# Kernel tuning notes

Hardware: AMD Instinct MI355X
Metric: run time of the kernel (lower is better)

Reference implementation:

```python
import jax, jax.numpy as jnp
import numpy as np

B, T, D, H, L, E, K, FF, V = 2, 1024, 1024, 16, 3, 8, 2, 4096, 32000
HD = D // H


def _rmsnorm(x):
    return x * jax.lax.rsqrt(jnp.mean(x * x, axis=-1, keepdims=True) + 1e-5)


def _forward(idx, wte, wpe, wq, wk, wv, wo, gate, f1, f2, lm_head):
    Bc, Tc = idx.shape
    x = wte[idx] + wpe[:Tc]            # (B,T,D)
    x = _rmsnorm(x)
    causal = jnp.tril(jnp.ones((Tc, Tc), dtype=bool))
    total_aux = jnp.zeros((), dtype=x.dtype)
    scale = 1.0 / np.sqrt(HD)
    for l in range(L):
        xr = x
        xn = _rmsnorm(x)
        q = (xn @ wq[l].T).reshape(Bc, Tc, H, HD).transpose(0, 2, 1, 3)
        k = (xn @ wk[l].T).reshape(Bc, Tc, H, HD).transpose(0, 2, 1, 3)
        v = (xn @ wv[l].T).reshape(Bc, Tc, H, HD).transpose(0, 2, 1, 3)
        att = jnp.einsum('bhqd,bhkd->bhqk', q, k) * scale
        att = jnp.where(causal, att, -jnp.inf)
        att = jax.nn.softmax(att, axis=-1)
        o = jnp.einsum('bhqk,bhkd->bhqd', att, v)
        o = o.transpose(0, 2, 1, 3).reshape(Bc, Tc, D)
        x = o @ wo[l].T + xr
        # MoE FFN (dense compute over all experts, gather top-k)
        xr = x
        xn = _rmsnorm(x)
        gate_probs = jax.nn.softmax(jnp.einsum('btd,ed->bte', xn, gate[l]), axis=-1)
        topk_vals, topk_idx = jax.lax.top_k(gate_probs, K)   # (B,T,K)
        topk_w = topk_vals / topk_vals.sum(axis=-1, keepdims=True)
        h = jax.nn.relu(jnp.einsum('btd,efd->btef', xn, f1[l]))  # (B,T,E,FF)
        expert_stack = jnp.einsum('btef,edf->bted', h, f2[l])    # (B,T,E,D)
        selected = jnp.take_along_axis(expert_stack, topk_idx[..., None], axis=2)  # (B,T,K,D)
        moe_out = (selected * topk_w[..., None]).sum(axis=2)
        frac = gate_probs.mean(axis=(0, 1))
        total_aux = total_aux + E * jnp.sum(frac * frac)
        x = moe_out + xr
    logits = x @ lm_head.T              # (B,T,V)
    aux_loss = 0.01 * total_aux / L
    return logits, aux_loss


def setup_inputs() -> dict:
    key = jax.random.key(0)
    ks = jax.random.split(key, 12)
    s = 0.02
    return {
        'idx': jax.random.randint(ks[0], (B, T), 0, V, dtype=jnp.int64) if jax.config.jax_enable_x64 else jax.random.randint(ks[0], (B, T), 0, V, dtype=jnp.int32),
        'wte': jax.random.normal(ks[1], (V, D), jnp.float32) * s,
        'wpe': jax.random.normal(ks[2], (T, D), jnp.float32) * s,
        'wq': jax.random.normal(ks[3], (L, D, D), jnp.float32) * s,
        'wk': jax.random.normal(ks[4], (L, D, D), jnp.float32) * s,
        'wv': jax.random.normal(ks[5], (L, D, D), jnp.float32) * s,
        'wo': jax.random.normal(ks[6], (L, D, D), jnp.float32) * s,
        'gate': jax.random.normal(ks[7], (L, E, D), jnp.float32) * s,
        'f1': jax.random.normal(ks[8], (L, E, FF, D), jnp.float32) * s,
        'f2': jax.random.normal(ks[9], (L, E, D, FF), jnp.float32) * s,
        'lm_head': jax.random.normal(ks[10], (V, D), jnp.float32) * s,
    }


def reference(idx, wte, wpe, wq, wk, wv, wo, gate, f1, f2, lm_head):
    return _forward(idx, wte, wpe, wq, wk, wv, wo, gate, f1, f2, lm_head)
```

## Files before the change

kernel.cpp:

```cpp
#include <hip/hip_runtime.h>

typedef unsigned short u16;
typedef __attribute__((ext_vector_type(4))) float f32x4;
typedef __attribute__((ext_vector_type(8))) __bf16 bf16x8;
typedef __attribute__((ext_vector_type(8))) _Float16 f16x8;
typedef __attribute__((ext_vector_type(4))) unsigned short u16x4;
typedef __attribute__((ext_vector_type(8))) unsigned short u16x8;

constexpr int kT = 1024, kD = 1024, kH = 16, kHD = 64, kL = 3, kE = 8;
constexpr int kFF = 4096, kV = 32000, kBT = 2048, kSLOTS = 5120;

__device__ __forceinline__ u16 f2bf(float f) {
  union { float f; unsigned u; } v; v.f = f;
  unsigned r = v.u + 0x7FFFu + ((v.u >> 16) & 1u);
  return (u16)(r >> 16);
}
__device__ __forceinline__ u16 f2h(float x) {
  _Float16 h = (_Float16)x;
  union { _Float16 h; u16 u; } v; v.h = h; return v.u;
}
__device__ __forceinline__ void split2s(float x, u16& h, u16& m) {
  float xs = x * 64.0f;
  _Float16 hh = (_Float16)xs;
  union { _Float16 h; u16 u; } v; v.h = hh; h = v.u;
  float r = xs - (float)hh;
  union { _Float16 h; u16 u; } w; w.h = (_Float16)r; m = w.u;
}

__device__ __forceinline__ void ld_lds16(const void* g, void* l) {
  __builtin_amdgcn_global_load_lds((const __attribute__((address_space(1))) void*)g,
                                   (__attribute__((address_space(3))) void*)l, 16, 0, 0);
}

#define MFMA16(a, b, c) __builtin_amdgcn_mfma_f32_16x16x32_bf16(a, b, c, 0, 0, 0)
#define MFMAH(a, b, c)  __builtin_amdgcn_mfma_f32_16x16x32_f16(a, b, c, 0, 0, 0)

__device__ __forceinline__ float blockReduceSum256(float v) {
  #pragma unroll
  for (int m = 32; m >= 1; m >>= 1) v += __shfl_xor(v, m);
  __shared__ float sh_[4];
  int w = threadIdx.x >> 6;
  if ((threadIdx.x & 63) == 0) sh_[w] = v;
  __syncthreads();
  v = (sh_[0] + sh_[1]) + (sh_[2] + sh_[3]);
  __syncthreads();
  return v;
}


__global__ __launch_bounds__(256) void cast_bf16_k(const float* __restrict__ in,
                                                   u16* __restrict__ out, long n4) {
  long i = (long)blockIdx.x * 256 + threadIdx.x;
  long stride = (long)gridDim.x * 256;
  for (; i < n4; i += stride) {
    f32x4 v = ((const f32x4*)in)[i];
    u16x4 o; o[0] = f2bf(v[0]); o[1] = f2bf(v[1]); o[2] = f2bf(v[2]); o[3] = f2bf(v[3]);
    ((u16x4*)out)[i] = o;
  }
}

__global__ __launch_bounds__(256) void cast_h_k(const float* __restrict__ in,
                                                u16* __restrict__ out, long n4) {
  long i = (long)blockIdx.x * 256 + threadIdx.x;
  long stride = (long)gridDim.x * 256;
  for (; i < n4; i += stride) {
    f32x4 v = ((const f32x4*)in)[i];
    u16x4 o; o[0] = f2h(v[0]); o[1] = f2h(v[1]); o[2] = f2h(v[2]); o[3] = f2h(v[3]);
    ((u16x4*)out)[i] = o;
  }
}

__global__ __launch_bounds__(256) void split2h_k(const float* __restrict__ in,
    u16* __restrict__ out, long planeStride, long n4) {
  long i = (long)blockIdx.x * 256 + threadIdx.x;
  long stride = (long)gridDim.x * 256;
  u16* o1 = out + planeStride;
  for (; i < n4; i += stride) {
    f32x4 v = ((const f32x4*)in)[i];
    u16x4 a, b;
    #pragma unroll
    for (int j = 0; j < 4; ++j) {
      u16 h, m; split2s(v[j], h, m);
      a[j] = h; b[j] = m;
    }
    ((u16x4*)out)[i] = a; ((u16x4*)o1)[i] = b;
  }
}

__global__ __launch_bounds__(256) void qkvcomb_k(const float* __restrict__ a,
    const float* __restrict__ b, u16* __restrict__ oP, long plane, long n4) {
  long i = (long)blockIdx.x * 256 + threadIdx.x;
  long stride = (long)gridDim.x * 256;
  for (; i < n4; i += stride) {
    f32x4 v = ((const f32x4*)a)[i] + ((const f32x4*)b)[i];
    u16x4 hh, mm;
    #pragma unroll
    for (int j = 0; j < 4; ++j) {
      u16 h, m; split2s(v[j], h, m);
      hh[j] = h; mm[j] = m;
    }
    ((u16x4*)oP)[i] = hh;
    ((u16x4*)(oP + plane))[i] = mm;
  }
}

__global__ __launch_bounds__(256) void embed_rms_k(const int* __restrict__ idx,
    const float* __restrict__ wte, const float* __restrict__ wpe, float* __restrict__ x) {
  int tok = blockIdx.x, t = threadIdx.x;
  int id = idx[tok];
  int tt = tok & (kT - 1);
  f32x4 a = ((const f32x4*)(wte + (long)id * kD))[t];
  f32x4 p = ((const f32x4*)(wpe + (long)tt * kD))[t];
  f32x4 vv = a + p;
  float ss = vv[0]*vv[0] + vv[1]*vv[1] + vv[2]*vv[2] + vv[3]*vv[3];
  ss = blockReduceSum256(ss);
  float sc = rsqrtf(ss * (1.0f / kD) + 1e-5f);
  vv *= sc;
  ((f32x4*)(x + (long)tok * kD))[t] = vv;
}

__global__ __launch_bounds__(256) void rmsnorm2_k(const float* __restrict__ x,
    float* __restrict__ xnf, u16* __restrict__ xnb) {
  int tok = blockIdx.x, t = threadIdx.x;
  f32x4 vv = ((const f32x4*)(x + (long)tok * kD))[t];
  float ss = blockReduceSum256(vv[0]*vv[0] + vv[1]*vv[1] + vv[2]*vv[2] + vv[3]*vv[3]);
  float sc = rsqrtf(ss * (1.0f / kD) + 1e-5f);
  vv *= sc;
  ((f32x4*)(xnf + (long)tok * kD))[t] = vv;
  u16x4 o;
  o[0] = f2bf(vv[0]); o[1] = f2bf(vv[1]); o[2] = f2bf(vv[2]); o[3] = f2bf(vv[3]);
  ((u16x4*)(xnb + (long)tok * kD))[t] = o;
}

__global__ __launch_bounds__(256) void rmsnorm2h_k(const float* __restrict__ x,
    u16* __restrict__ xnP, long plane) {
  int tok = blockIdx.x, t = threadIdx.x;
  f32x4 vv = ((const f32x4*)(x + (long)tok * kD))[t];
  float ss = blockReduceSum256(vv[0]*vv[0] + vv[1]*vv[1] + vv[2]*vv[2] + vv[3]*vv[3]);
  float sc = rsqrtf(ss * (1.0f / kD) + 1e-5f);
  vv *= sc;
  u16x4 a, b;
  #pragma unroll
  for (int j = 0; j < 4; ++j) {
    u16 h, m; split2s(vv[j], h, m);
    a[j] = h; b[j] = m;
  }
  long o = (long)tok * kD / 4 + t;
  ((u16x4*)xnP)[o] = a;
  ((u16x4*)(xnP + plane))[o] = b;
}

__global__ __launch_bounds__(256) void resid4_rms2h_k(float* __restrict__ x,
    const float* __restrict__ parts, long plane, u16* __restrict__ xnP, long xplane) {
  int tok = blockIdx.x, t = threadIdx.x;
  long o = (long)tok * (kD / 4) + t;
  f32x4 xv = ((f32x4*)x)[o];
  #pragma unroll
  for (int p = 0; p < 4; ++p) xv += ((const f32x4*)(parts + p * plane))[o];
  ((f32x4*)x)[o] = xv;
  float ss = blockReduceSum256(xv[0]*xv[0] + xv[1]*xv[1] + xv[2]*xv[2] + xv[3]*xv[3]);
  float sc = rsqrtf(ss * (1.0f / kD) + 1e-5f);
  f32x4 vv = xv * sc;
  u16x4 a, b;
  #pragma unroll
  for (int j = 0; j < 4; ++j) {
    u16 h, m; split2s(vv[j], h, m);
    a[j] = h; b[j] = m;
  }
  ((u16x4*)xnP)[o] = a;
  ((u16x4*)(xnP + xplane))[o] = b;
}

__global__ __launch_bounds__(256) void moe4_rms2h_k(float* __restrict__ x,
    const float* __restrict__ outsP, long plane, const int* __restrict__ slotOf,
    const float* __restrict__ top2w, u16* __restrict__ xnP, long xplane) {
  int tok = blockIdx.x, t = threadIdx.x;
  int s0 = slotOf[tok*2], s1 = slotOf[tok*2+1];
  float w0 = top2w[tok*2], w1 = top2w[tok*2+1];
  f32x4 a = {0.f,0.f,0.f,0.f}, b = a;
  #pragma unroll
  for (int p = 0; p < 4; ++p) {
    a += ((const f32x4*)(outsP + p * plane + (long)s0 * kD))[t];
    b += ((const f32x4*)(outsP + p * plane + (long)s1 * kD))[t];
  }
  long o = (long)tok * (kD / 4) + t;
  f32x4 xv = ((f32x4*)x)[o];
  xv += a * w0 + b * w1;
  ((f32x4*)x)[o] = xv;
  float ss = blockReduceSum256(xv[0]*xv[0] + xv[1]*xv[1] + xv[2]*xv[2] + xv[3]*xv[3]);
  float sc = rsqrtf(ss * (1.0f / kD) + 1e-5f);
  f32x4 vv = xv * sc;
  u16x4 ha, hb;
  #pragma unroll
  for (int j = 0; j < 4; ++j) {
    u16 h, m; split2s(vv[j], h, m);
    ha[j] = h; hb[j] = m;
  }
  ((u16x4*)xnP)[o] = ha;
  ((u16x4*)(xnP + xplane))[o] = hb;
}

__global__ __launch_bounds__(256) void moe4_cast_h_k(float* __restrict__ x,
    const float* __restrict__ outsP, long plane, const int* __restrict__ slotOf,
    const float* __restrict__ top2w, u16* __restrict__ xn) {
  int tok = blockIdx.x, t = threadIdx.x;
  int s0 = slotOf[tok*2], s1 = slotOf[tok*2+1];
  float w0 = top2w[tok*2], w1 = top2w[tok*2+1];
  f32x4 a = {0.f,0.f,0.f,0.f}, b = a;
  #pragma unroll
  for (int p = 0; p < 4; ++p) {
    a += ((const f32x4*)(outsP + p * plane + (long)s0 * kD))[t];
    b += ((const f32x4*)(outsP + p * plane + (long)s1 * kD))[t];
  }
  long o = (long)tok * (kD / 4) + t;
  f32x4 xv = ((f32x4*)x)[o];
  xv += a * w0 + b * w1;
  u16x4 hv;
  #pragma unroll
  for (int j = 0; j < 4; ++j) hv[j] = f2h(xv[j]);
  ((u16x4*)xn)[o] = hv;
}

__global__ __launch_bounds__(256) void gate_topk_k(const float* __restrict__ x,
    const float* __restrict__ gate_l, float* __restrict__ probs, int* __restrict__ top2e,
    float* __restrict__ top2w, int* __restrict__ counts) {
  int tok = blockIdx.x, t = threadIdx.x;
  f32x4 xv = ((const f32x4*)(x + (long)tok * kD))[t];
  float ss = blockReduceSum256(xv[0]*xv[0] + xv[1]*xv[1] + xv[2]*xv[2] + xv[3]*xv[3]);
  float sc = rsqrtf(ss * (1.0f / kD) + 1e-5f);
  float a[kE];
  #pragma unroll
  for (int e = 0; e < kE; ++e) {
    f32x4 gv = ((const f32x4*)(gate_l + (long)e * kD))[t];
    a[e] = xv[0]*gv[0] + xv[1]*gv[1] + xv[2]*gv[2] + xv[3]*gv[3];
  }
  __shared__ float sh8[kE][4];
  int w = t >> 6, l = t & 63;
  #pragma unroll
  for (int e = 0; e < kE; ++e) {
    float v = a[e];
    #pragma unroll
    for (int m = 32; m >= 1; m >>= 1) v += __shfl_xor(v, m);
    if (l == 0) sh8[e][w] = v;
  }
  __syncthreads();
  if (t == 0) {
    float lg[kE], mx = -1e30f;
    #pragma unroll
    for (int e = 0; e < kE; ++e) {
      lg[e] = (sh8[e][0] + sh8[e][1] + sh8[e][2] + sh8[e][3]) * sc;
      mx = fmaxf(mx, lg[e]);
    }
    float pe[kE], s = 0.f;
    #pragma unroll
    for (int e = 0; e < kE; ++e) { pe[e] = __expf(lg[e] - mx); s += pe[e]; }
    float inv = 1.f / s;
    int i1 = 0;
    #pragma unroll
    for (int e = 1; e < kE; ++e) if (lg[e] > lg[i1]) i1 = e;
    int i2 = (i1 == 0) ? 1 : 0;
    #pragma unroll
    for (int e = 0; e < kE; ++e) if (e != i1 && lg[e] > lg[i2]) i2 = e;
    #pragma unroll
    for (int e = 0; e < kE; ++e) probs[(long)tok * kE + e] = pe[e] * inv;
    float p1 = pe[i1] * inv, p2 = pe[i2] * inv;
    float wn = p1 + p2;
    top2e[tok*2] = i1; top2e[tok*2+1] = i2;
    top2w[tok*2] = p1 / wn; top2w[tok*2+1] = p2 / wn;
    atomicAdd(&counts[i1], 1); atomicAdd(&counts[i2], 1);
  }
}

__global__ void calc_offsets_k(const int* __restrict__ counts, int* __restrict__ offsets) {
  if (threadIdx.x == 0) {
    int o = 0;
    #pragma unroll
    for (int e = 0; e < kE; ++e) { offsets[e] = o; o += (counts[e] + 127) & ~127; }
    offsets[kE] = o;
  }
}

__global__ __launch_bounds__(256) void fill_slots_k(const int* __restrict__ top2e,
    const int* __restrict__ offsets, int* __restrict__ cursors,
    int* __restrict__ rows, int* __restrict__ slotOf) {
  int tok = blockIdx.x * 256 + threadIdx.x;
  if (tok >= kBT) return;
  #pragma unroll
  for (int j = 0; j < 2; ++j) {
    int e = top2e[tok*2 + j];
    int pos = atomicAdd(&cursors[e], 1);
    int slot = offsets[e] + pos;
    rows[slot] = tok;
    slotOf[tok*2 + j] = slot;
  }
}

__global__ __launch_bounds__(256) void moe_combine4_k(float* __restrict__ x,
    const float* __restrict__ outsP, long plane, const int* __restrict__ slotOf,
    const float* __restrict__ top2w) {
  int tok = blockIdx.x, t = threadIdx.x;
  int s0 = slotOf[tok*2], s1 = slotOf[tok*2+1];
  float w0 = top2w[tok*2], w1 = top2w[tok*2+1];
  f32x4 a = {0.f,0.f,0.f,0.f}, b = a;
  #pragma unroll
  for (int p = 0; p < 4; ++p) {
    a += ((const f32x4*)(outsP + p * plane + (long)s0 * kD))[t];
    b += ((const f32x4*)(outsP + p * plane + (long)s1 * kD))[t];
  }
  f32x4 xv = ((f32x4*)(x + (long)tok * kD))[t];
  xv += a * w0 + b * w1;
  ((f32x4*)(x + (long)tok * kD))[t] = xv;
}

__global__ __launch_bounds__(256) void aux_reduce_k(const float* __restrict__ probs,
                                                    float* __restrict__ aux) {
  int t = threadIdx.x;
  float part[kE] = {};
  for (int i = t; i < kBT; i += 256) {
    #pragma unroll
    for (int e = 0; e < kE; ++e) part[e] += probs[(long)i * kE + e];
  }
  __shared__ float sh8[kE][4];
  int w = t >> 6, l = t & 63;
  #pragma unroll
  for (int e = 0; e < kE; ++e) {
    float v = part[e];
    #pragma unroll
    for (int m = 32; m >= 1; m >>= 1) v += __shfl_xor(v, m);
    if (l == 0) sh8[e][w] = v;
  }
  __syncthreads();
  if (t == 0) {
    float acc = 0.f;
    #pragma unroll
    for (int e = 0; e < kE; ++e) {
      float frac = (sh8[e][0] + sh8[e][1] + sh8[e][2] + sh8[e][3]) * (1.0f / kBT);
      acc += frac * frac;
    }
    aux[0] += (float)kE * acc;
  }
}

__global__ void write_aux_k(const float* __restrict__ aux, float* __restrict__ out) {
  if (threadIdx.x == 0) out[0] = 0.01f * aux[0] / (float)kL;
}

enum { P_BF16 = 0, P_BF16_RELU = 1, P_F32 = 2, P_F32_RESID = 3, P_F32_RELU = 4,
       P_SPLIT2_RELU = 5, P_F16_RELU = 6 };

__device__ __forceinline__ int clamp_row(int rv) {
  return ((unsigned)rv < (unsigned)kBT) ? rv : 0;
}

template <bool MPART>
__device__ __forceinline__ void block_mn(int lin, int base, int mArg, int& mb, int& nb) {
  int xcd = lin & 7, c = lin >> 3;
  if (MPART) {
    mb = xcd * mArg + (c % mArg);
    nb = c / mArg;
  } else {
    int swz = xcd * (base >> 3) + c;
    mb = swz % mArg;
    nb = swz / mArg;
  }
}


template <int POST, bool GATHER, bool EXPERT, bool MPART, bool BF32>
__global__ __launch_bounds__(256) void gemm2h_bt_k(
    const u16* __restrict__ A0, long planeA,
    const void* __restrict__ Bv, long planeB,
    void* __restrict__ C, long planeC,
    const float* __restrict__ resid,
    const int* __restrict__ rows, const int* __restrict__ offsets,
    int N, int K, int lda, long eBstride, int mArg,
    int kParts, int base, long cPart) {
  constexpr int BM = 128, BK = 32;
  int part = blockIdx.x / base;
  int lin = blockIdx.x % base;
  int mb, nb;
  block_mn<MPART>(lin, base, mArg, mb, nb);
  int m0 = mb * BM, n0 = nb * BM;
  const u16* B0 = (const u16*)Bv;
  const float* Bf = (const float*)Bv;
  if (EXPERT) {
    int total = offsets[kE];
    if (m0 >= total) return;
    int e = 0;
    while (offsets[e + 1] <= m0) ++e;
    if (BF32) Bf += (long)e * eBstride; else B0 += (long)e * eBstride;
  }
  __shared__ __align__(16) u16 Ac[BM][64];
  __shared__ __align__(16) u16 Bc[BM][64];
  int t = threadIdx.x;
  int l = t & 63, lr = l & 15, lg = l >> 4;
  int wid = t >> 6;
  int wm = (wid >> 1) * 64, wn = (wid & 1) * 64;

  long asrc[4], bsrc[4];
  int ldst[4];
  #pragma unroll
  for (int it = 0; it < 4; ++it) {
    int d = it * 256 + t;
    int row = d >> 3, pc = d & 7;
    int lc = pc ^ (row & 7);
    int p = lc >> 2, c = lc & 3;
    int grow = GATHER ? clamp_row(rows[m0 + row]) : (m0 + row);
    asrc[it] = (long)p * planeA + (long)grow * lda + c * 8;
    if (!BF32) bsrc[it] = (long)p * planeB + (long)(n0 + row) * K + c * 8;
    ldst[it] = (it * 256 + (t & ~63)) * 8;
  }
  long bsrcF[2];
  int brow[2], bc[2];
  if (BF32) {
    #pragma unroll
    for (int it = 0; it < 2; ++it) {
      int d = it * 256 + t;
      brow[it] = d >> 2; bc[it] = d & 3;
      bsrcF[it] = (long)(n0 + brow[it]) * K + bc[it] * 8;
    }
  }
  int sa = lr & 7;
  int cH = (lg ^ sa) * 8;
  int cM = ((4 + lg) ^ sa) * 8;

  f32x4 acc[4][4];
  #pragma unroll
  for (int i = 0; i < 4; ++i)
    #pragma unroll
    for (int j = 0; j < 4; ++j) acc[i][j] = 0.f;

  int kStep = K / kParts;
  int kLo = part * kStep, kHi = kLo + kStep;
  for (int k0 = kLo; k0 < kHi; k0 += BK) {
    #pragma unroll
    for (int it = 0; it < 4; ++it) {
      ld_lds16(A0 + asrc[it] + k0, &Ac[0][0] + ldst[it]);
      if (!BF32) ld_lds16(B0 + bsrc[it] + k0, &Bc[0][0] + ldst[it]);
    }
    if (BF32) {
      #pragma unroll
      for (int it = 0; it < 2; ++it) {
        const float* src = Bf + bsrcF[it] + k0;
        f32x4 v0 = *(const f32x4*)src;
        f32x4 v1 = *(const f32x4*)(src + 4);
        u16x8 hi, mi;
        #pragma unroll
        for (int j = 0; j < 4; ++j) {
          u16 h, m; split2s(v0[j], h, m); hi[j] = h; mi[j] = m;
        }
        #pragma unroll
        for (int j = 0; j < 4; ++j) {
          u16 h, m; split2s(v1[j], h, m); hi[4 + j] = h; mi[4 + j] = m;
        }
        int r7 = brow[it] & 7;
        *(u16x8*)&Bc[brow[it]][(bc[it] ^ r7) * 8] = hi;
        *(u16x8*)&Bc[brow[it]][((4 + bc[it]) ^ r7) * 8] = mi;
      }
    }
    __syncthreads();
    f16x8 ah[4], am[4];
    #pragma unroll
    for (int i = 0; i < 4; ++i) {
      ah[i] = *(const f16x8*)&Ac[wm + i*16 + lr][cH];
      am[i] = *(const f16x8*)&Ac[wm + i*16 + lr][cM];
    }
    #pragma unroll
    for (int j = 0; j < 4; ++j) {
      f16x8 bh = *(const f16x8*)&Bc[wn + j*16 + lr][cH];
      f16x8 bm = *(const f16x8*)&Bc[wn + j*16 + lr][cM];
      #pragma unroll
      for (int i = 0; i < 4; ++i) {
        acc[i][j] = MFMAH(ah[i], bh, acc[i][j]);
        acc[i][j] = MFMAH(am[i], bh, acc[i][j]);
        acc[i][j] = MFMAH(ah[i], bm, acc[i][j]);
      }
    }
    __syncthreads();
  }
  float* Cf = (float*)C + (long)part * cPart;
  #pragma unroll
  for (int i = 0; i < 4; ++i) {
    #pragma unroll
    for (int r = 0; r < 4; ++r) {
      long m = m0 + wm + i*16 + lg*4 + r;
      #pragma unroll
      for (int j = 0; j < 4; ++j) {
        int n = n0 + wn + j*16 + lr;
        float val = acc[i][j][r] * (1.0f / 4096.0f);
        if (POST == P_F32) {
          Cf[m * N + n] = val;
        } else if (POST == P_F32_RESID) {
          ((float*)C)[m * N + n] = val + resid[m * N + n];
        } else if (POST == P_SPLIT2_RELU) {
          val = fmaxf(val, 0.f);
          u16 h, mm; split2s(val, h, mm);
          u16* Cp = (u16*)C;
          Cp[m * N + n] = h;
          Cp[planeC + m * N + n] = mm;
        }
      }
    }
  }
}


template <int POST, bool GATHER, bool EXPERT, bool BF32>
__global__ __launch_bounds__(512) void gemm2hW_bt_k(
    const u16* __restrict__ A0, long planeA,
    const void* __restrict__ Bv, long planeB,
    void* __restrict__ C, long planeC,
    const int* __restrict__ rows, const int* __restrict__ offsets,
    int N, int K, int lda, long eBstride, int mPerX,
    int kParts, int base, long cPart) {
  constexpr int BM = 128, BN = 256, BK = 32;
  int part = blockIdx.x / base;
  int lin = blockIdx.x % base;
  int xcd = lin & 7, c0 = lin >> 3;
  int m0 = (xcd * mPerX + (c0 % mPerX)) * BM;
  int n0 = (c0 / mPerX) * BN;
  const u16* B0 = (const u16*)Bv;
  const float* Bf = (const float*)Bv;
  if (EXPERT) {
    int total = offsets[kE];
    if (m0 >= total) return;
    int e = 0;
    while (offsets[e + 1] <= m0) ++e;
    if (BF32) Bf += (long)e * eBstride; else B0 += (long)e * eBstride;
  }
  __shared__ __align__(16) u16 Ac[BM][64];
  __shared__ __align__(16) u16 Bc[BN][64];
  int t = threadIdx.x;
  int l = t & 63, lr = l & 15, lg = l >> 4;
  int wid = t >> 6;
  int wm = (wid >> 2) * 64;
  int wn = (wid & 3) * 64;

  long asrc[2], bsrc[4];
  int aldst[2], bldst[4];
  #pragma unroll
  for (int it = 0; it < 2; ++it) {
    int d = it * 512 + t;
    int row = d >> 3, pc = d & 7;
    int lc = pc ^ (row & 7);
    int p = lc >> 2, cc = lc & 3;
    int grow = GATHER ? clamp_row(rows[m0 + row]) : (m0 + row);
    asrc[it] = (long)p * planeA + (long)grow * lda + cc * 8;
    aldst[it] = (it * 512 + (t & ~63)) * 8;
  }
  long bsrcF[2];
  int brow[2], bcc[2];
  if (!BF32) {
    #pragma unroll
    for (int it = 0; it < 4; ++it) {
      int d = it * 512 + t;
      int row = d >> 3, pc = d & 7;
      int lc = pc ^ (row & 7);
      int p = lc >> 2, cc = lc & 3;
      bsrc[it] = (long)p * planeB + (long)(n0 + row) * K + cc * 8;
      bldst[it] = (it * 512 + (t & ~63)) * 8;
    }
  } else {
    #pragma unroll
    for (int it = 0; it < 2; ++it) {
      int d = it * 512 + t;
      brow[it] = d >> 2; bcc[it] = d & 3;
      bsrcF[it] = (long)(n0 + brow[it]) * K + bcc[it] * 8;
    }
  }
  int sa = lr & 7;
  int cH = (lg ^ sa) * 8;
  int cM = ((4 + lg) ^ sa) * 8;

  f32x4 acc[4][4];
  #pragma unroll
  for (int i = 0; i < 4; ++i)
    #pragma unroll
    for (int j = 0; j < 4; ++j) acc[i][j] = 0.f;

  int kStep = K / kParts;
  int kLo = part * kStep, kHi = kLo + kStep;
  for (int k0 = kLo; k0 < kHi; k0 += BK) {
    #pragma unroll
    for (int it = 0; it < 2; ++it)
      ld_lds16(A0 + asrc[it] + k0, &Ac[0][0] + aldst[it]);
    if (!BF32) {
      #pragma unroll
      for (int it = 0; it < 4; ++it)
        ld_lds16(B0 + bsrc[it] + k0, &Bc[0][0] + bldst[it]);
    } else {
      #pragma unroll
      for (int it = 0; it < 2; ++it) {
        const float* src = Bf + bsrcF[it] + k0;
        f32x4 v0 = *(const f32x4*)src;
        f32x4 v1 = *(const f32x4*)(src + 4);
        u16x8 hi, mi;
        #pragma unroll
        for (int j = 0; j < 4; ++j) {
          u16 h, m; split2s(v0[j], h, m); hi[j] = h; mi[j] = m;
        }
        #pragma unroll
        for (int j = 0; j < 4; ++j) {
          u16 h, m; split2s(v1[j], h, m); hi[4 + j] = h; mi[4 + j] = m;
        }
        int r7 = brow[it] & 7;
        *(u16x8*)&Bc[brow[it]][(bcc[it] ^ r7) * 8] = hi;
        *(u16x8*)&Bc[brow[it]][((4 + bcc[it]) ^ r7) * 8] = mi;
      }
    }
    __syncthreads();
    f16x8 ah[4], am[4];
    #pragma unroll
    for (int i = 0; i < 4; ++i) {
      ah[i] = *(const f16x8*)&Ac[wm + i*16 + lr][cH];
      am[i] = *(const f16x8*)&Ac[wm + i*16 + lr][cM];
    }
    #pragma unroll
    for (int j = 0; j < 4; ++j) {
      f16x8 bh = *(const f16x8*)&Bc[wn + j*16 + lr][cH];
      f16x8 bm = *(const f16x8*)&Bc[wn + j*16 + lr][cM];
      #pragma unroll
      for (int i = 0; i < 4; ++i) {
        acc[i][j] = MFMAH(ah[i], bh, acc[i][j]);
        acc[i][j] = MFMAH(am[i], bh, acc[i][j]);
        acc[i][j] = MFMAH(ah[i], bm, acc[i][j]);
      }
    }
    __syncthreads();
  }
  float* Cf = (float*)C + (long)part * cPart;
  #pragma unroll
  for (int i = 0; i < 4; ++i) {
    #pragma unroll
    for (int r = 0; r < 4; ++r) {
      long m = m0 + wm + i*16 + lg*4 + r;
      #pragma unroll
      for (int j = 0; j < 4; ++j) {
        int n = n0 + wn + j*16 + lr;
        float val = acc[i][j][r] * (1.0f / 4096.0f);
        if (POST == P_F32) {
          Cf[m * N + n] = val;
        } else if (POST == P_SPLIT2_RELU) {
          val = fmaxf(val, 0.f);
          u16 h, mm; split2s(val, h, mm);
          u16* Cp = (u16*)C;
          Cp[m * N + n] = h;
          Cp[planeC + m * N + n] = mm;
        }
      }
    }
  }
}


template <int POST, bool EXPERT, bool GATHER, bool HALF, bool BCONV, bool MPART>
__global__ __launch_bounds__(256) void gemm_bt_k(
    const u16* __restrict__ A, const void* __restrict__ Bv, void* __restrict__ C,
    const int* __restrict__ rows, const int* __restrict__ offsets,
    int N, int K, int lda, long eBstride, float oscale, int mArg,
    int kParts, int base, long cPart) {
  constexpr int BM = 128, BK = 64;
  int part = blockIdx.x / base;
  int lin = blockIdx.x % base;
  int mb, nb;
  block_mn<MPART>(lin, base, mArg, mb, nb);
  int m0 = mb * BM, n0 = nb * BM;
  const float* Bf = (const float*)Bv;
  const u16*   Bh = (const u16*)Bv;
  if (EXPERT) {
    int total = offsets[kE];
    if (m0 >= total) return;
    int e = 0;
    while (offsets[e + 1] <= m0) ++e;
    if (BCONV) Bf += (long)e * eBstride; else Bh += (long)e * eBstride;
  }
  __shared__ __align__(16) u16 As[BM][BK];
  __shared__ __align__(16) u16 Bs[BM][BK + (BCONV ? 8 : 0)];
  int t = threadIdx.x;
  int l = t & 63, lr = l & 15, lg = l >> 4;
  int wid = t >> 6;
  int wm = (wid >> 1) * 64, wn = (wid & 1) * 64;

  long asrc[4], bsrc[4];
  int ldst[4];
  #pragma unroll
  for (int it = 0; it < 4; ++it) {
    int d = it * 256 + t;
    int row = d >> 3, pc = d & 7;
    int c = pc ^ (row & 7);
    int grow = GATHER ? clamp_row(rows[m0 + row]) : (m0 + row);
    asrc[it] = (long)grow * lda + c * 8;
    bsrc[it] = (long)(n0 + row) * K + c * 8;
    ldst[it] = (it * 256 + (t & ~63)) * 8;
  }
  f32x4 acc[4][4];
  #pragma unroll
  for (int i = 0; i < 4; ++i)
    #pragma unroll
    for (int j = 0; j < 4; ++j) acc[i][j] = 0.f;

  int kStep = K / kParts;
  int kLo = part * kStep, kHi = kLo + kStep;
  for (int k0 = kLo; k0 < kHi; k0 += BK) {
    #pragma unroll
    for (int it = 0; it < 4; ++it)
      ld_lds16(A + asrc[it] + k0, &As[0][0] + ldst[it]);
    if (!BCONV) {
      #pragma unroll
      for (int it = 0; it < 4; ++it)
        ld_lds16(Bh + bsrc[it] + k0, &Bs[0][0] + ldst[it]);
    } else {
      #pragma unroll
      for (int it = 0; it < 8; ++it) {
        int c = it * 256 + t;
        int row = c >> 4, col = (c & 15) * 4;
        f32x4 v = *(const f32x4*)(Bf + (long)(n0 + row) * K + k0 + col);
        u16x4 o;
        #pragma unroll
        for (int j = 0; j < 4; ++j) o[j] = HALF ? f2h(v[j]) : f2bf(v[j]);
        *(u16x4*)&Bs[row][col] = o;
      }
    }
    __syncthreads();
    #pragma unroll
    for (int kk = 0; kk < 2; ++kk) {
      int ca = ((kk * 4 + lg) ^ (lr & 7)) * 8;
      int cb = BCONV ? (kk * 32 + lg * 8) : ca;
      #pragma unroll
      for (int i = 0; i < 4; ++i)
        #pragma unroll
        for (int j = 0; j < 4; ++j) {
          if (HALF) {
            f16x8 af = *(const f16x8*)&As[wm + i*16 + lr][ca];
            f16x8 bq = *(const f16x8*)&Bs[wn + j*16 + lr][cb];
            acc[i][j] = MFMAH(af, bq, acc[i][j]);
          } else {
            bf16x8 af = *(const bf16x8*)&As[wm + i*16 + lr][ca];
            bf16x8 bq = *(const bf16x8*)&Bs[wn + j*16 + lr][cb];
            acc[i][j] = MFMA16(af, bq, acc[i][j]);
          }
        }
    }
    __syncthreads();
  }
  #pragma unroll
  for (int i = 0; i < 4; ++i) {
    #pragma unroll
    for (int r = 0; r < 4; ++r) {
      long m = m0 + wm + i*16 + lg*4 + r;
      #pragma unroll
      for (int j = 0; j < 4; ++j) {
        int n = n0 + wn + j*16 + lr;
        float val = acc[i][j][r] * oscale;
        if (POST == P_BF16_RELU)       ((u16*)C)[m * N + n] = f2bf(fmaxf(val, 0.f));
        else if (POST == P_F16_RELU)   ((u16*)C)[m * N + n] = f2h(fmaxf(val, 0.f));
        else if (POST == P_F32)        ((float*)C + (long)part * cPart)[m * N + n] = val;
      }
    }
  }
}


template <int POST, bool GATHER, bool EXPERT>
__global__ __launch_bounds__(256) void sgemm_bt_k(
    const float* __restrict__ A, const float* __restrict__ B, float* __restrict__ C,
    const float* __restrict__ resid, const int* __restrict__ rows,
    const int* __restrict__ offsets, int N, int K, int lda, long eBstride) {
  constexpr int BM = 128, BN = 128, BK = 32;
  int m0 = blockIdx.x * BM, n0 = blockIdx.y * BN;
  if (EXPERT) {
    int total = offsets[kE];
    if (m0 >= total) return;
    int e = 0;
    while (offsets[e + 1] <= m0) ++e;
    B += (long)e * eBstride;
  }
  __shared__ float Ast[BK][BM];
  __shared__ float Bst[BK][BN];
  int t = threadIdx.x, tx = t & 15, ty = t >> 4;
  long asrc[4], bsrc[4];
  #pragma unroll
  for (int it = 0; it < 4; ++it) {
    int c = it * 256 + t;
    int row = c >> 3, kc = (c & 7) * 4;
    int gr = GATHER ? clamp_row(rows[m0 + row]) : (m0 + row);
    asrc[it] = (long)gr * lda + kc;
    bsrc[it] = (long)(n0 + row) * K + kc;
  }
  f32x4 accv[8][2];
  #pragma unroll
  for (int i = 0; i < 8; ++i) { accv[i][0] = 0.f; accv[i][1] = 0.f; }

  for (int k0 = 0; k0 < K; k0 += BK) {
    #pragma unroll
    for (int it = 0; it < 4; ++it) {
      int c = it * 256 + t;
      int row = c >> 3, kc = (c & 7) * 4;
      f32x4 av = *(const f32x4*)(A + asrc[it] + k0);
      f32x4 bv = *(const f32x4*)(B + bsrc[it] + k0);
      #pragma unroll
      for (int j = 0; j < 4; ++j) { Ast[kc + j][row] = av[j]; Bst[kc + j][row] = bv[j]; }
    }
    __syncthreads();
    #pragma unroll
    for (int kk = 0; kk < BK; ++kk) {
      f32x4 a0 = *(const f32x4*)&Ast[kk][ty * 4];
      f32x4 a1 = *(const f32x4*)&Ast[kk][64 + ty * 4];
      f32x4 b0 = *(const f32x4*)&Bst[kk][tx * 4];
      f32x4 b1 = *(const f32x4*)&Bst[kk][64 + tx * 4];
      float as[8] = {a0[0], a0[1], a0[2], a0[3], a1[0], a1[1], a1[2], a1[3]};
      #pragma unroll
      for (int i = 0; i < 8; ++i) {
        accv[i][0] += b0 * as[i];
        accv[i][1] += b1 * as[i];
      }
    }
    __syncthreads();
  }
  #pragma unroll
  for (int ih = 0; ih < 2; ++ih)
    #pragma unroll
    for (int i = 0; i < 4; ++i) {
      long m = m0 + ih * 64 + ty * 4 + i;
      #pragma unroll
      for (int jh = 0; jh < 2; ++jh) {
        long n = n0 + jh * 64 + tx * 4;
        f32x4 val = accv[ih * 4 + i][jh];
        if (POST == P_F32_RELU) {
          #pragma unroll
          for (int j = 0; j < 4; ++j) val[j] = fmaxf(val[j], 0.f);
        }
        if (POST == P_F32_RESID) val += *(const f32x4*)&resid[m * N + n];
        *(f32x4*)&C[m * N + n] = val;
      }
    }
}


__global__ __launch_bounds__(256) void attn2h_k(
    const u16* __restrict__ qkvP, long qplane,
    u16* __restrict__ oP, long oplane) {
  int qt = (int)gridDim.x - 1 - (int)blockIdx.x;
  int bh = blockIdx.y;
  int b = bh >> 4, h = bh & 15;
  const int ldq = 3 * kD;
  long hbq = (long)b * kT * ldq + h * kHD;
  long hbo = (long)b * kT * kD + h * kHD;
  int t = threadIdx.x, w = t >> 6, l = t & 63;
  int lr = l & 15, lg = l >> 4;

  __shared__ __align__(16) u16 Ks[2][64][72];
  __shared__ __align__(16) u16 Vt[2][64][72];
  __shared__ __align__(16) u16 Ps[2][4][16][72];

  f16x8 qf0[2], qf1[2];
  {
    long qrow = qt * 64 + w * 16 + lr;
    const u16* qp = qkvP + hbq + qrow * ldq;
    #pragma unroll
    for (int kc = 0; kc < 2; ++kc) {
      qf0[kc] = *(const f16x8*)(qp + kc * 32 + lg * 8);
      qf1[kc] = *(const f16x8*)(qp + qplane + kc * 32 + lg * 8);
    }
  }
  int qg = qt * 64 + w * 16 + lg * 4;

  float mrow[4], lsum[4];
  f32x4 accO[4];
  #pragma unroll
  for (int r = 0; r < 4; ++r) { mrow[r] = -1e30f; lsum[r] = 0.f; }
  #pragma unroll
  for (int j = 0; j < 4; ++j) accO[j] = 0.f;

  for (int it = 0; it <= qt; ++it) {
    #pragma unroll
    for (int p = 0; p < 2; ++p) {
      #pragma unroll
      for (int s = 0; s < 2; ++s) {
        int c = s * 256 + t;
        int row = c >> 3, col = (c & 7) * 8;
        long gi = (long)p * qplane + hbq + (long)(it * 64 + row) * ldq + col;
        *(u16x8*)&Ks[p][row][col] = *(const u16x8*)(qkvP + kD + gi);
        u16x8 vv = *(const u16x8*)(qkvP + 2 * kD + gi);
        #pragma unroll
        for (int j = 0; j < 8; ++j) Vt[p][col + j][row] = vv[j];
      }
    }
    __syncthreads();

    f32x4 s4[4];
    #pragma unroll
    for (int j = 0; j < 4; ++j) {
      f32x4 z = {0.f, 0.f, 0.f, 0.f};
      #pragma unroll
      for (int kc = 0; kc < 2; ++kc) {
        f16x8 kh = *(const f16x8*)&Ks[0][j*16 + lr][kc*32 + lg*8];
        f16x8 km = *(const f16x8*)&Ks[1][j*16 + lr][kc*32 + lg*8];
        z = MFMAH(qf0[kc], kh, z);
        z = MFMAH(qf1[kc], kh, z);
        z = MFMAH(qf0[kc], km, z);
      }
      s4[j] = z;
    }
    #pragma unroll
    for (int j = 0; j < 4; ++j)
      #pragma unroll
      for (int r = 0; r < 4; ++r) {
        float sv = s4[j][r] * (0.125f / 4096.0f);
        if (it * 64 + j * 16 + lr > qg + r) sv = -1e30f;
        s4[j][r] = sv;
      }
    float alpha[4];
    #pragma unroll
    for (int r = 0; r < 4; ++r) {
      float mx = fmaxf(fmaxf(s4[0][r], s4[1][r]), fmaxf(s4[2][r], s4[3][r]));
      mx = fmaxf(mx, __shfl_xor(mx, 1));
      mx = fmaxf(mx, __shfl_xor(mx, 2));
      mx = fmaxf(mx, __shfl_xor(mx, 4));
      mx = fmaxf(mx, __shfl_xor(mx, 8));
      float mi = fmaxf(mrow[r], mx);
      alpha[r] = __expf(mrow[r] - mi);
      mrow[r] = mi;
    }
    float rs[4] = {0.f, 0.f, 0.f, 0.f};
    #pragma unroll
    for (int j = 0; j < 4; ++j)
      #pragma unroll
      for (int r = 0; r < 4; ++r) {
        float p = __expf(s4[j][r] - mrow[r]);
        rs[r] += p;
        u16 hh, mm; split2s(p, hh, mm);
        Ps[0][w][lg*4 + r][j*16 + lr] = hh;
        Ps[1][w][lg*4 + r][j*16 + lr] = mm;
      }
    #pragma unroll
    for (int r = 0; r < 4; ++r) {
      float x2 = rs[r];
      x2 += __shfl_xor(x2, 1);
      x2 += __shfl_xor(x2, 2);
      x2 += __shfl_xor(x2, 4);
      x2 += __shfl_xor(x2, 8);
      lsum[r] = lsum[r] * alpha[r] + x2;
    }
    #pragma unroll
    for (int j = 0; j < 4; ++j)
      #pragma unroll
      for (int r = 0; r < 4; ++r) accO[j][r] *= alpha[r];
    __syncthreads();

    f16x8 ph[2], pm[2];
    #pragma unroll
    for (int kc = 0; kc < 2; ++kc) {
      ph[kc] = *(const f16x8*)&Ps[0][w][lr][kc*32 + lg*8];
      pm[kc] = *(const f16x8*)&Ps[1][w][lr][kc*32 + lg*8];
    }
    #pragma unroll
    for (int j2 = 0; j2 < 4; ++j2) {
      #pragma unroll
      for (int kc = 0; kc < 2; ++kc) {
        f16x8 vh = *(const f16x8*)&Vt[0][j2*16 + lr][kc*32 + lg*8];
        f16x8 vm = *(const f16x8*)&Vt[1][j2*16 + lr][kc*32 + lg*8];
        accO[j2] = MFMAH(ph[kc], vh, accO[j2]);
        accO[j2] = MFMAH(pm[kc], vh, accO[j2]);
        accO[j2] = MFMAH(ph[kc], vm, accO[j2]);
      }
    }
    __syncthreads();
  }
  #pragma unroll
  for (int j2 = 0; j2 < 4; ++j2)
    #pragma unroll
    for (int r = 0; r < 4; ++r) {
      float ov = accO[j2][r] * (1.0f / 4096.0f) / lsum[r];
      long row = qt * 64 + w * 16 + lg * 4 + r;
      long idx = hbo + row * kD + j2 * 16 + lr;
      u16 hh, mm; split2s(ov, hh, mm);
      oP[idx] = hh;
      oP[oplane + idx] = mm;
    }
}


__global__ __launch_bounds__(256) void attn_f32_k(
    const float* __restrict__ qkv, float* __restrict__ of32, int ldq) {
  int qt = blockIdx.x;
  int bh = blockIdx.y;
  int b = bh >> 4, h = bh & 15;
  long hbq = (long)b * kT * ldq + h * kHD;
  long hbo = (long)b * kT * kD + h * kHD;
  int t = threadIdx.x, qr = t >> 2, sub = t & 3;

  __shared__ float Qs[64][68], Ks[64][68], Vs[64][68], Ps[64][68];

  const float* q = qkv;
  const float* k = qkv + kD;
  const float* v = qkv + 2 * kD;

  #pragma unroll
  for (int it = 0; it < 4; ++it) {
    int c = it * 256 + t, row = c >> 4, c4 = (c & 15) * 4;
    f32x4 qv = *(const f32x4*)(q + hbq + (long)(qt * 64 + row) * ldq + c4);
    #pragma unroll
    for (int j = 0; j < 4; ++j) Qs[row][c4 + j] = qv[j];
  }
  __syncthreads();
  f32x4 qreg[16];
  #pragma unroll
  for (int d4 = 0; d4 < 16; ++d4) qreg[d4] = *(const f32x4*)&Qs[qr][d4 * 4];
  int qg = qt * 64 + qr;

  float mrow = -1e30f, lsum = 0.f;
  f32x4 accO[4];
  #pragma unroll
  for (int i = 0; i < 4; ++i) accO[i] = 0.f;

  for (int itl = 0; itl <= qt; ++itl) {
    #pragma unroll
    for (int it = 0; it < 4; ++it) {
      int c = it * 256 + t, row = c >> 4, c4 = (c & 15) * 4;
      long gi = hbq + (long)(itl * 64 + row) * ldq + c4;
      f32x4 kv = *(const f32x4*)(k + gi);
      f32x4 vv = *(const f32x4*)(v + gi);
      #pragma unroll
      for (int j = 0; j < 4; ++j) { Ks[row][c4 + j] = kv[j]; Vs[row][c4 + j] = vv[j]; }
    }
    __syncthreads();

    float s[16];
    #pragma unroll
    for (int kk = 0; kk < 16; ++kk) {
      int key = kk * 4 + sub;
      f32x4 a = {0.f, 0.f, 0.f, 0.f};
      #pragma unroll
      for (int d4 = 0; d4 < 16; ++d4) a += qreg[d4] * *(const f32x4*)&Ks[key][d4 * 4];
      float sv = (a[0] + a[1] + a[2] + a[3]) * 0.125f;
      if (itl * 64 + key > qg) sv = -1e30f;
      s[kk] = sv;
    }
    float mx = s[0];
    #pragma unroll
    for (int kk = 1; kk < 16; ++kk) mx = fmaxf(mx, s[kk]);
    mx = fmaxf(mx, __shfl_xor(mx, 1));
    mx = fmaxf(mx, __shfl_xor(mx, 2));
    float mi = fmaxf(mrow, mx);
    float alpha = __expf(mrow - mi);
    mrow = mi;
    float rs = 0.f;
    #pragma unroll
    for (int kk = 0; kk < 16; ++kk) {
      float p = __expf(s[kk] - mi);
      rs += p;
      Ps[qr][kk * 4 + sub] = p;
    }
    rs += __shfl_xor(rs, 1);
    rs += __shfl_xor(rs, 2);
    lsum = lsum * alpha + rs;
    #pragma unroll
    for (int i = 0; i < 4; ++i) accO[i] *= alpha;
    #pragma unroll
    for (int key2 = 0; key2 < 64; ++key2) {
      float p = Ps[qr][key2];
      #pragma unroll
      for (int i4 = 0; i4 < 4; ++i4)
        accO[i4] += p * *(const f32x4*)&Vs[key2][sub * 16 + i4 * 4];
    }
    __syncthreads();
  }
  float inv = 1.f / lsum;
  #pragma unroll
  for (int i4 = 0; i4 < 4; ++i4) {
    f32x4 ov = accO[i4] * inv;
    *(f32x4*)(of32 + hbo + (long)qg * kD + sub * 16 + i4 * 4) = ov;
  }
}


extern "C" void kernel_launch(void* const* d_in, const int* in_sizes, int n_in,
                              void* d_out, int out_size, void* d_ws, size_t ws_size,
                              hipStream_t stream) {
  const int*   idx  = (const int*)  d_in[0];
  const float* wte  = (const float*)d_in[1];
  const float* wpe  = (const float*)d_in[2];
  const float* wq   = (const float*)d_in[3];
  const float* wk   = (const float*)d_in[4];
  const float* wv   = (const float*)d_in[5];
  const float* wo   = (const float*)d_in[6];
  const float* gate = (const float*)d_in[7];
  const float* f1   = (const float*)d_in[8];
  const float* f2   = (const float*)d_in[9];
  const float* lmh  = (const float*)d_in[10];
  float* out = (float*)d_out;

  char* ws = (char*)d_ws;
  size_t off = 0;
  auto alloc = [&](size_t b) -> char* {
    char* p = ws + off;
    off += (b + 255) & ~(size_t)255;
    return p;
  };

  constexpr long PLN_XN = (long)kBT * kD;
  constexpr long PLN_Q3 = (long)kBT * 3 * kD;
  constexpr long PLN_QKV = (long)3 * kD * kD;
  constexpr long PLN_WO = (long)kD * kD;
  constexpr long PLN_FF = (long)kE * kFF * kD;
  constexpr long PLN_H = (long)kSLOTS * kFF;
  constexpr long PLN_OUTS = (long)kSLOTS * kD;

  float* x     = (float*)alloc((size_t)kBT * kD * 4);
  float* outs  = (float*)alloc((size_t)4 * PLN_OUTS * 4);
  float* probs = (float*)alloc((size_t)kBT * kE * 4);
  int*   top2e = (int*)  alloc((size_t)kBT * 2 * 4);
  float* top2w = (float*)alloc((size_t)kBT * 2 * 4);
  int*   meta  = (int*)  alloc(64 * 4);
  int* counts = meta; int* cursors = meta + 8; int* offs = meta + 16;
  int*   rows  = (int*)  alloc((size_t)kSLOTS * 4);
  int*   slotOf= (int*)  alloc((size_t)kBT * 2 * 4);
  float* aux   = (float*)alloc(256);
  size_t off_shared = off;

  u16*   xnP   = (u16*)  alloc((size_t)2 * PLN_XN * 2);
  float* qkvf  = (float*)alloc((size_t)PLN_Q3 * 4);
  u16*   qkvP  = (u16*)  alloc((size_t)2 * PLN_Q3 * 2);
  u16*   ofP   = (u16*)  alloc((size_t)2 * PLN_XN * 2);
  u16*   hP    = (u16*)  alloc((size_t)2 * PLN_H * 2);
  u16*   wqkvP = (u16*)  alloc((size_t)kL * 2 * PLN_QKV * 2);
  u16*   woP   = (u16*)  alloc((size_t)kL * 2 * PLN_WO * 2);
  bool fast = (off <= ws_size);
  float* qkvp1 = (float*)hP;

  dim3 gAttn(kT / 64, 2 * kH);
  int bQKV = (kBT / 128) * (3 * kD / 128);
  int bWO  = (kBT / 128) * (kD / 128);
  int nF1W = (kSLOTS / 128) * (kFF / 256);
  int bF2  = (kSLOTS / 128) * (kD / 128);
  int nF1s = (kSLOTS / 128) * (kFF / 128);
  int nLM  = (kBT / 128) * (kV / 128);

  if (fast) {
    for (int li = 0; li < kL; ++li) {
      u16* dst = wqkvP + (size_t)li * 2 * PLN_QKV;
      split2h_k<<<1024, 256, 0, stream>>>(wq + (size_t)li * kD * kD, dst, PLN_QKV, (long)kD * kD / 4);
      split2h_k<<<1024, 256, 0, stream>>>(wk + (size_t)li * kD * kD, dst + (long)kD * kD, PLN_QKV, (long)kD * kD / 4);
      split2h_k<<<1024, 256, 0, stream>>>(wv + (size_t)li * kD * kD, dst + (long)2 * kD * kD, PLN_QKV, (long)kD * kD / 4);
      split2h_k<<<1024, 256, 0, stream>>>(wo + (size_t)li * kD * kD, woP + (size_t)li * 2 * PLN_WO, PLN_WO, (long)kD * kD / 4);
    }
    hipMemsetAsync(aux, 0, 4, stream);
    embed_rms_k<<<kBT, 256, 0, stream>>>(idx, wte, wpe, x);
    rmsnorm2h_k<<<kBT, 256, 0, stream>>>(x, xnP, PLN_XN);

    for (int li = 0; li < kL; ++li) {
      gemm2h_bt_k<P_F32, false, false, true, false><<<2 * bQKV, 256, 0, stream>>>(
          xnP, PLN_XN, wqkvP + (size_t)li * 2 * PLN_QKV, PLN_QKV,
          qkvf, 0, nullptr, nullptr, nullptr, 3 * kD, kD, kD, 0, 2,
          2, bQKV, (long)(qkvp1 - qkvf));
      qkvcomb_k<<<2048, 256, 0, stream>>>(qkvf, qkvp1, qkvP, PLN_Q3, PLN_Q3 / 4);
      attn2h_k<<<gAttn, 256, 0, stream>>>(qkvP, PLN_Q3, ofP, PLN_XN);
      gemm2h_bt_k<P_F32, false, false, true, false><<<4 * bWO, 256, 0, stream>>>(
          ofP, PLN_XN, woP + (size_t)li * 2 * PLN_WO, PLN_WO,
          outs, 0, nullptr, nullptr, nullptr, kD, kD, kD, 0, 2,
          4, bWO, PLN_OUTS);
      resid4_rms2h_k<<<kBT, 256, 0, stream>>>(x, outs, PLN_OUTS, xnP, PLN_XN);
      hipMemsetAsync(meta, 0, 64, stream);
      gate_topk_k<<<kBT, 256, 0, stream>>>(x, gate + (size_t)li * kE * kD,
                                           probs, top2e, top2w, counts);
      calc_offsets_k<<<1, 64, 0, stream>>>(counts, offs);
      fill_slots_k<<<kBT / 256, 256, 0, stream>>>(top2e, offs, cursors, rows, slotOf);
      size_t fd = (size_t)li * PLN_FF;
      if (li < 2) {
        gemm2hW_bt_k<P_SPLIT2_RELU, true, true, true><<<nF1W, 512, 0, stream>>>(
            xnP, PLN_XN, f1 + fd, 0, hP, PLN_H, rows, offs,
            kFF, kD, kD, (long)kFF * kD, kSLOTS / 128 / 8,
            1, nF1W, 0);
        gemm2h_bt_k<P_F32, false, true, true, true><<<4 * bF2, 256, 0, stream>>>(
            hP, PLN_H, f2 + fd, 0, outs, 0, nullptr, nullptr, offs,
            kD, kFF, kFF, (long)kD * kFF, kSLOTS / 128 / 8,
            4, bF2, PLN_OUTS);
        moe4_rms2h_k<<<kBT, 256, 0, stream>>>(x, outs, PLN_OUTS, slotOf, top2w,
                                              xnP, PLN_XN);
      } else {
        gemm_bt_k<P_F16_RELU, true, true, true, true, true><<<nF1s, 256, 0, stream>>>(
            xnP, f1 + fd, hP, rows, offs, kFF, kD, kD, (long)kFF * kD,
            1.0f / 64.0f, kSLOTS / 128 / 8, 1, nF1s, 0);
        gemm_bt_k<P_F32, true, false, true, true, true><<<4 * bF2, 256, 0, stream>>>(
            hP, f2 + fd, outs, nullptr, offs, kD, kFF, kFF, (long)kD * kFF,
            1.0f, kSLOTS / 128 / 8, 4, bF2, PLN_OUTS);
        moe4_cast_h_k<<<kBT, 256, 0, stream>>>(x, outs, PLN_OUTS, slotOf, top2w, xnP);
      }
      aux_reduce_k<<<1, 256, 0, stream>>>(probs, aux);
    }
    gemm_bt_k<P_F32, false, false, true, true, false><<<nLM, 256, 0, stream>>>(
        xnP, lmh, out, nullptr, nullptr, kV, kD, kD, 0, 1.0f, kBT / 128,
        1, nLM, 0);
    write_aux_k<<<1, 64, 0, stream>>>(aux, out + (size_t)kBT * kV);
    return;
  }

  off = off_shared;
  float* xnf   = (float*)alloc((size_t)kBT * kD * 4);
  u16*   xnb   = (u16*)  alloc((size_t)kBT * kD * 2);
  float* qkvf32= (float*)alloc((size_t)kBT * 3 * kD * 4);
  float* off32 = (float*)alloc((size_t)kBT * kD * 4);
  float* hbuf  = (float*)alloc((size_t)kSLOTS * kFF * 4);
  u16* hbuf16 = (u16*)hbuf;

  hipMemsetAsync(aux, 0, 4, stream);
  embed_rms_k<<<kBT, 256, 0, stream>>>(idx, wte, wpe, x);
  dim3 gF1s(kSLOTS / 128, kFF / 128);
  dim3 gF2s(kSLOTS / 128, kD / 128);
  for (int li = 0; li < kL; ++li) {
    size_t dd = (size_t)li * kD * kD;
    rmsnorm2_k<<<kBT, 256, 0, stream>>>(x, xnf, xnb);
    dim3 gP(kBT / 128, kD / 128);
    sgemm_bt_k<P_F32, false, false><<<gP, 256, 0, stream>>>(
        xnf, wq + dd, qkvf32, nullptr, nullptr, nullptr, 3 * kD, kD, kD, 0);
    sgemm_bt_k<P_F32, false, false><<<gP, 256, 0, stream>>>(
        xnf, wk + dd, qkvf32 + kD, nullptr, nullptr, nullptr, 3 * kD, kD, kD, 0);
    sgemm_bt_k<P_F32, false, false><<<gP, 256, 0, stream>>>(
        xnf, wv + dd, qkvf32 + 2 * kD, nullptr, nullptr, nullptr, 3 * kD, kD, kD, 0);
    attn_f32_k<<<gAttn, 256, 0, stream>>>(qkvf32, off32, 3 * kD);
    sgemm_bt_k<P_F32_RESID, false, false><<<gP, 256, 0, stream>>>(
        off32, wo + dd, x, x, nullptr, nullptr, kD, kD, kD, 0);
    rmsnorm2_k<<<kBT, 256, 0, stream>>>(x, xnf, xnb);
    hipMemsetAsync(meta, 0, 64, stream);
    gate_topk_k<<<kBT, 256, 0, stream>>>(x, gate + (size_t)li * kE * kD,
                                         probs, top2e, top2w, counts);
    calc_offsets_k<<<1, 64, 0, stream>>>(counts, offs);
    fill_slots_k<<<kBT / 256, 256, 0, stream>>>(top2e, offs, cursors, rows, slotOf);
    size_t fd = (size_t)li * kE * kFF * kD;
    if (li < 2) {
      sgemm_bt_k<P_F32_RELU, true, true><<<gF1s, 256, 0, stream>>>(
          xnf, f1 + fd, hbuf, nullptr, rows, offs, kFF, kD, kD, (long)kFF * kD);
      sgemm_bt_k<P_F32, false, true><<<gF2s, 256, 0, stream>>>(
          hbuf, f2 + fd, outs, nullptr, nullptr, offs, kD, kFF, kFF, (long)kD * kFF);
    } else {
      gemm_bt_k<P_BF16_RELU, true, true, false, true, false><<<nF1s, 256, 0, stream>>>(
          xnb, f1 + fd, hbuf16, rows, offs, kFF, kD, kD, (long)kFF * kD,
          1.0f, kSLOTS / 128, 1, nF1s, 0);
      gemm_bt_k<P_F32, true, false, false, true, false><<<bF2, 256, 0, stream>>>(
          hbuf16, f2 + fd, outs, nullptr, offs, kD, kFF, kFF, (long)kD * kFF,
          1.0f, kSLOTS / 128, 1, bF2, 0);
    }
    hipMemsetAsync(outs + PLN_OUTS, 0, 3 * PLN_OUTS * 4, stream);
    moe_combine4_k<<<kBT, 256, 0, stream>>>(x, outs, PLN_OUTS, slotOf, top2w);
    aux_reduce_k<<<1, 256, 0, stream>>>(probs, aux);
  }
  cast_bf16_k<<<2048, 256, 0, stream>>>(x, xnb, (long)kBT * kD / 4);
  gemm_bt_k<P_F32, false, false, false, true, false><<<nLM, 256, 0, stream>>>(
      xnb, lmh, out, nullptr, nullptr, kV, kD, kD, 0, 1.0f, kBT / 128,
      1, nLM, 0);
  write_aux_k<<<1, 64, 0, stream>>>(aux, out + (size_t)kBT * kV);
}
```

Before: 2.076 ms.

## Pre-cast lm_head to fp16 and swizzle converted B tiles in LDS

The LM-head GEMM used to convert fp32 weights to fp16 inside every block. It now runs on an fp16 copy made once by a separate cast kernel, so it takes the direct async LDS-load path. The in-kernel B-conversion path, still used by the MoE fallback, now writes 8-wide XOR-swizzled rows instead of padded rows. This lets both A and B share the same swizzled read index, cutting LDS bank conflicts. The cost is an extra 64 MB-read cast pass over lm_head on every call, plus extra workspace.

```diff
diff --git a/kernel.cpp b/kernel.cpp
--- a/kernel.cpp
+++ b/kernel.cpp
@@ -675,7 +675,7 @@
     if (BCONV) Bf += (long)e * eBstride; else Bh += (long)e * eBstride;
   }
   __shared__ __align__(16) u16 As[BM][BK];
-  __shared__ __align__(16) u16 Bs[BM][BK + (BCONV ? 8 : 0)];
+  __shared__ __align__(16) u16 Bs[BM][BK];
   int t = threadIdx.x;
   int l = t & 63, lr = l & 15, lg = l >> 4;
   int wid = t >> 6;
@@ -690,8 +690,19 @@
     int c = pc ^ (row & 7);
     int grow = GATHER ? clamp_row(rows[m0 + row]) : (m0 + row);
     asrc[it] = (long)grow * lda + c * 8;
-    bsrc[it] = (long)(n0 + row) * K + c * 8;
+    if (!BCONV) bsrc[it] = (long)(n0 + row) * K + c * 8;
     ldst[it] = (it * 256 + (t & ~63)) * 8;
+  }
+  long bsrcC[4];
+  int bdst[4];
+  if (BCONV) {
+    #pragma unroll
+    for (int it = 0; it < 4; ++it) {
+      int d = it * 256 + t;
+      int row = d >> 3, lc = d & 7;
+      bsrcC[it] = (long)(n0 + row) * K + lc * 8;
+      bdst[it] = row * BK + (lc ^ (row & 7)) * 8;
+    }
   }
   f32x4 acc[4][4];
   #pragma unroll
@@ -711,32 +722,34 @@
         ld_lds16(Bh + bsrc[it] + k0, &Bs[0][0] + ldst[it]);
     } else {
       #pragma unroll
-      for (int it = 0; it < 8; ++it) {
-        int c = it * 256 + t;
-        int row = c >> 4, col = (c & 15) * 4;
-        f32x4 v = *(const f32x4*)(Bf + (long)(n0 + row) * K + k0 + col);
-        u16x4 o;
+      for (int it = 0; it < 4; ++it) {
+        const float* src = Bf + bsrcC[it] + k0;
+        f32x4 v0 = *(const f32x4*)src;
+        f32x4 v1 = *(const f32x4*)(src + 4);
+        u16x8 o;
         #pragma unroll
-        for (int j = 0; j < 4; ++j) o[j] = HALF ? f2h(v[j]) : f2bf(v[j]);
-        *(u16x4*)&Bs[row][col] = o;
+        for (int j = 0; j < 4; ++j) {
+          o[j] = HALF ? f2h(v0[j]) : f2bf(v0[j]);
+          o[4 + j] = HALF ? f2h(v1[j]) : f2bf(v1[j]);
+        }
+        *(u16x8*)(&Bs[0][0] + bdst[it]) = o;
       }
     }
     __syncthreads();
     #pragma unroll
     for (int kk = 0; kk < 2; ++kk) {
       int ca = ((kk * 4 + lg) ^ (lr & 7)) * 8;
-      int cb = BCONV ? (kk * 32 + lg * 8) : ca;
       #pragma unroll
       for (int i = 0; i < 4; ++i)
         #pragma unroll
         for (int j = 0; j < 4; ++j) {
           if (HALF) {
             f16x8 af = *(const f16x8*)&As[wm + i*16 + lr][ca];
-            f16x8 bq = *(const f16x8*)&Bs[wn + j*16 + lr][cb];
+            f16x8 bq = *(const f16x8*)&Bs[wn + j*16 + lr][ca];
             acc[i][j] = MFMAH(af, bq, acc[i][j]);
           } else {
             bf16x8 af = *(const bf16x8*)&As[wm + i*16 + lr][ca];
-            bf16x8 bq = *(const bf16x8*)&Bs[wn + j*16 + lr][cb];
+            bf16x8 bq = *(const bf16x8*)&Bs[wn + j*16 + lr][ca];
             acc[i][j] = MFMA16(af, bq, acc[i][j]);
           }
         }
@@ -1126,6 +1139,7 @@
   u16*   hP    = (u16*)  alloc((size_t)2 * PLN_H * 2);
   u16*   wqkvP = (u16*)  alloc((size_t)kL * 2 * PLN_QKV * 2);
   u16*   woP   = (u16*)  alloc((size_t)kL * 2 * PLN_WO * 2);
+  u16*   lmb   = (u16*)  alloc((size_t)kV * kD * 2);
   bool fast = (off <= ws_size);
   float* qkvp1 = (float*)hP;
 
@@ -1145,6 +1159,7 @@
       split2h_k<<<1024, 256, 0, stream>>>(wv + (size_t)li * kD * kD, dst + (long)2 * kD * kD, PLN_QKV, (long)kD * kD / 4);
       split2h_k<<<1024, 256, 0, stream>>>(wo + (size_t)li * kD * kD, woP + (size_t)li * 2 * PLN_WO, PLN_WO, (long)kD * kD / 4);
     }
+    cast_h_k<<<4096, 256, 0, stream>>>(lmh, lmb, (long)kV * kD / 4);
     hipMemsetAsync(aux, 0, 4, stream);
     embed_rms_k<<<kBT, 256, 0, stream>>>(idx, wte, wpe, x);
     rmsnorm2h_k<<<kBT, 256, 0, stream>>>(x, xnP, PLN_XN);
@@ -1189,8 +1204,8 @@
       }
       aux_reduce_k<<<1, 256, 0, stream>>>(probs, aux);
     }
-    gemm_bt_k<P_F32, false, false, true, true, false><<<nLM, 256, 0, stream>>>(
-        xnP, lmh, out, nullptr, nullptr, kV, kD, kD, 0, 1.0f, kBT / 128,
+    gemm_bt_k<P_F32, false, false, true, false, false><<<nLM, 256, 0, stream>>>(
+        xnP, lmb, out, nullptr, nullptr, kV, kD, kD, 0, 1.0f, kBT / 128,
         1, nLM, 0);
     write_aux_k<<<1, 64, 0, stream>>>(aux, out + (size_t)kBT * kV);
     return;
```

After: 2.027 ms. -2.4%, faster.
